# Kernel tuning notes

Measured on AMD Instinct MI355X. Metric: run time of the kernel, lower is better.

Reference implementation:

```python
import jax, jax.numpy as jnp
import numpy as np

N = 100000      # nodes
F_IN = 512      # input features
H = 128         # hidden
C = 16          # classes
E = 3200000     # edges
K = 10          # propagation hops (lg_k == gg_k == 10)
ALPHA = 0.1


def ppr_temp(K, alpha):
    t = alpha * (1.0 - alpha) ** np.arange(K + 1)
    t[-1] = (1.0 - alpha) ** K
    return jnp.asarray(t, dtype=jnp.float32)


def setup_inputs() -> dict:
    key = jax.random.key(0)
    ks = jax.random.split(key, 8)
    x = jax.random.normal(ks[0], (N, F_IN), dtype=jnp.float32)
    edge_index = jax.random.randint(ks[1], (2, E), 0, N, dtype=jnp.int64)
    # Local branch: kaiming-uniform-ish linears
    W1_l = jax.random.uniform(ks[2], (F_IN, H), jnp.float32, -1.0, 1.0) * np.sqrt(6.0 / F_IN)
    b1_l = jnp.zeros((H,), jnp.float32)
    W2_l = jax.random.uniform(ks[3], (H, C), jnp.float32, -1.0, 1.0) * np.sqrt(6.0 / H)
    b2_l = jnp.zeros((C,), jnp.float32)
    temp_l = ppr_temp(K, ALPHA)
    # Global branch: uniform(-0.1, 0.1) linears
    W1_g = jax.random.uniform(ks[4], (F_IN, H), jnp.float32, -0.1, 0.1)
    b1_g = jnp.zeros((H,), jnp.float32)
    W2_g = jax.random.uniform(ks[5], (H, C), jnp.float32, -0.1, 0.1)
    b2_g = jnp.zeros((C,), jnp.float32)
    temp_g = ppr_temp(K, ALPHA)
    return {"x": x, "edge_index": edge_index,
            "W1_l": W1_l, "b1_l": b1_l, "W2_l": W2_l, "b2_l": b2_l, "temp_l": temp_l,
            "W1_g": W1_g, "b1_g": b1_g, "W2_g": W2_g, "b2_g": b2_g, "temp_g": temp_g}


def gpr_prop(x, edge_index, temp):
    # gcn_norm: add self-loops with weight 1, symmetric normalization
    row = jnp.concatenate([edge_index[0], jnp.arange(N, dtype=edge_index.dtype)])
    col = jnp.concatenate([edge_index[1], jnp.arange(N, dtype=edge_index.dtype)])
    deg = jax.ops.segment_sum(jnp.ones(row.shape[0], x.dtype), col, num_segments=N)
    dis = jnp.where(deg > 0, jax.lax.rsqrt(deg), 0.0).astype(x.dtype)
    norm = dis[row] * dis[col]  # [E+N]

    def step(carry, gamma):
        xc, hid = carry
        # gather-scale-scatter: out[col] += norm * xc[row]
        xn = jax.ops.segment_sum(norm[:, None] * xc[row], col, num_segments=N)
        return (xn, hid + gamma * xn), None

    (_, hidden), _ = jax.lax.scan(step, (x, x * temp[0]), temp[1:])
    return hidden


def gprgnn_branch(x, edge_index, W1, b1, W2, b2, temp):
    h1 = jax.nn.relu(x @ W1 + b1)          # [N, H]
    h2 = h1 @ W2 + b2                      # [N, C]
    h2 = gpr_prop(h2, edge_index, temp)    # K-hop GPR diffusion
    return h1, h2, jax.nn.log_softmax(h2, axis=1)


def reference(x, edge_index, W1_l, b1_l, W2_l, b2_l, temp_l,
              W1_g, b1_g, W2_g, b2_g, temp_g):
    h1_l, h2_l, prob_l = gprgnn_branch(x, edge_index, W1_l, b1_l, W2_l, b2_l, temp_l)
    h1_g, h2_g, prob_g = gprgnn_branch(x, edge_index, W1_g, b1_g, W2_g, b2_g, temp_g)
    return (h1_l, h2_l, prob_l, h1_g, h2_g, prob_g)
```

## Files before the change

kernel.cpp:

```cpp
#include <hip/hip_runtime.h>
#include <stdint.h>

#define F_IN 512
#define HDIM 128
#define CDIM 16
#define KHOPS 10

#define NBMAX 1024
#define CSTR 16
#define CHUNK 8192
#define CH2 32768

typedef __bf16 bf16x8 __attribute__((ext_vector_type(8)));
typedef float f32x4 __attribute__((ext_vector_type(4)));

typedef __attribute__((address_space(3))) unsigned int lds_uint;
typedef const __attribute__((address_space(1))) unsigned int g_uint;

__device__ __forceinline__ void dma16(const void* g, void* l) {
    __builtin_amdgcn_global_load_lds((g_uint*)g, (lds_uint*)l, 16, 0, 0);
}

__device__ __forceinline__ unsigned short f2bf(float f) {
    unsigned int u = __float_as_uint(f);
    u += 0x7FFFu + ((u >> 16) & 1u);
    return (unsigned short)(u >> 16);
}

__device__ __forceinline__ bf16x8 ld_bf8(const unsigned short* p) {
    uint4 u = *reinterpret_cast<const uint4*>(p);
    return __builtin_bit_cast(bf16x8, u);
}


__global__ __launch_bounds__(256) void k_ccount(const int* __restrict__ eidx,
                                                int* __restrict__ ccnt, int E) {
    __shared__ int lh[NBMAX];
    int t = threadIdx.x;
    int base = blockIdx.x * CH2;
    int lim = E - base; if (lim > CH2) lim = CH2;
    for (int i = t; i < NBMAX; i += 256) lh[i] = 0;
    __syncthreads();
    for (int j = t; j < lim; j += 256)
        atomicAdd(&lh[eidx[(size_t)E + base + j] >> 8], 1);
    __syncthreads();
    for (int i = t; i < NBMAX; i += 256) {
        int v = lh[i];
        if (v) atomicAdd(&ccnt[i], v);
    }
}

__global__ void k_cscan(const int* __restrict__ ccnt, int* __restrict__ coffs,
                        int* __restrict__ ccur, int nbuk) {
    __shared__ int sh[256];
    int t = threadIdx.x;
    int i0 = t * 4;
    int v0 = ccnt[i0 + 0], v1 = ccnt[i0 + 1], v2 = ccnt[i0 + 2], v3 = ccnt[i0 + 3];
    int s = v0 + v1 + v2 + v3;
    sh[t] = s;
    __syncthreads();
    for (int d = 1; d < 256; d <<= 1) {
        int x = (t >= d) ? sh[t - d] : 0;
        __syncthreads();
        sh[t] += x;
        __syncthreads();
    }
    int e0 = sh[t] - s;
    int e1 = e0 + v0, e2 = e1 + v1, e3 = e2 + v2;
    coffs[i0 + 0] = e0;
    coffs[i0 + 1] = e1;
    coffs[i0 + 2] = e2;
    coffs[i0 + 3] = e3;
    if (t == 255) coffs[1024] = e3 + v3;
    if (i0 + 0 < nbuk) ccur[(i0 + 0) * CSTR] = e0;
    if (i0 + 1 < nbuk) ccur[(i0 + 1) * CSTR] = e1;
    if (i0 + 2 < nbuk) ccur[(i0 + 2) * CSTR] = e2;
    if (i0 + 3 < nbuk) ccur[(i0 + 3) * CSTR] = e3;
}

__global__ __launch_bounds__(256) void k_part(
    const int* __restrict__ eidx, int* __restrict__ ccur,
    uint2* __restrict__ cedges, int E)
{
    __shared__ int lh[NBMAX];
    __shared__ int loff[NBMAX];
    __shared__ int lcur[NBMAX];
    __shared__ int gbase[NBMAX];
    __shared__ int sh[256];

    int t = threadIdx.x;
    int base = blockIdx.x * CHUNK;
    int lim = E - base; if (lim > CHUNK) lim = CHUNK;

    for (int i = t; i < NBMAX; i += 256) lh[i] = 0;
    __syncthreads();

    for (int j = t; j < lim; j += 256) {
        int c = eidx[(size_t)E + base + j];
        atomicAdd(&lh[c >> 8], 1);
    }
    __syncthreads();

    int i0 = t * 4;
    int v0 = lh[i0 + 0], v1 = lh[i0 + 1], v2 = lh[i0 + 2], v3 = lh[i0 + 3];
    int s = v0 + v1 + v2 + v3;
    sh[t] = s;
    __syncthreads();
    for (int d = 1; d < 256; d <<= 1) {
        int x = (t >= d) ? sh[t - d] : 0;
        __syncthreads();
        sh[t] += x;
        __syncthreads();
    }
    int excl = sh[t] - s;
    loff[i0 + 0] = excl; lcur[i0 + 0] = excl;
    gbase[i0 + 0] = v0 ? atomicAdd(&ccur[(i0 + 0) * CSTR], v0) : 0;
    excl += v0;
    loff[i0 + 1] = excl; lcur[i0 + 1] = excl;
    gbase[i0 + 1] = v1 ? atomicAdd(&ccur[(i0 + 1) * CSTR], v1) : 0;
    excl += v1;
    loff[i0 + 2] = excl; lcur[i0 + 2] = excl;
    gbase[i0 + 2] = v2 ? atomicAdd(&ccur[(i0 + 2) * CSTR], v2) : 0;
    excl += v2;
    loff[i0 + 3] = excl; lcur[i0 + 3] = excl;
    gbase[i0 + 3] = v3 ? atomicAdd(&ccur[(i0 + 3) * CSTR], v3) : 0;
    __syncthreads();

    for (int j = t; j < lim; j += 256) {
        int r = eidx[base + j];
        int c = eidx[(size_t)E + base + j];
        int b = c >> 8;
        int lp = atomicAdd(&lcur[b], 1);
        int gpos = gbase[b] + (lp - loff[b]);
        uint2 u; u.x = (unsigned)r; u.y = (unsigned)c;
        cedges[gpos] = u;
    }
}

__global__ __launch_bounds__(256) void k_fineA(
    const uint2* __restrict__ cedges, const int* __restrict__ coffs,
    int* __restrict__ cnt, float* __restrict__ dis, int* __restrict__ offs, int N)
{
    __shared__ int lh[256];
    __shared__ int sh[256];
    int b = blockIdx.x;
    int t = threadIdx.x;
    int col0 = b << 8;
    int segs = coffs[b];
    int sege = coffs[b + 1];
    lh[t] = 0;
    __syncthreads();
    for (int j = segs + t; j < sege; j += 256)
        atomicAdd(&lh[(int)cedges[j].y - col0], 1);
    __syncthreads();
    int c = lh[t];
    sh[t] = c;
    __syncthreads();
    for (int d = 1; d < 256; d <<= 1) {
        int x = (t >= d) ? sh[t - d] : 0;
        __syncthreads();
        sh[t] += x;
        __syncthreads();
    }
    int excl = sh[t] - c;
    int col = col0 + t;
    if (col < N) {
        cnt[col] = c;
        dis[col] = rsqrtf((float)(c + 1));
        offs[col] = segs + excl;
    }
}

__global__ __launch_bounds__(256) void k_fineB(
    const uint2* __restrict__ cedges, const int* __restrict__ coffs,
    const int* __restrict__ offs, int* __restrict__ srcs, int N)
{
    __shared__ int lcur[256];
    int b = blockIdx.x;
    int col0 = b << 8;
    int t = threadIdx.x;
    int col = col0 + t;
    int segs = coffs[b];
    int sege = coffs[b + 1];
    if (col < N) lcur[t] = offs[col];
    __syncthreads();
    for (int j = segs + t; j < sege; j += 256) {
        uint2 e = cedges[j];
        int li = (int)e.y - col0;
        int pos = atomicAdd(&lcur[li], 1);
        srcs[pos] = (int)e.x;
    }
}


__global__ void k_xbf(const float* __restrict__ x, unsigned short* __restrict__ xbf) {
    size_t i = (size_t)blockIdx.x * 2048 + (size_t)threadIdx.x * 8;
    float4 a = *reinterpret_cast<const float4*>(&x[i]);
    float4 b = *reinterpret_cast<const float4*>(&x[i + 4]);
    unsigned short s[8];
    s[0] = f2bf(a.x); s[1] = f2bf(a.y); s[2] = f2bf(a.z); s[3] = f2bf(a.w);
    s[4] = f2bf(b.x); s[5] = f2bf(b.y); s[6] = f2bf(b.z); s[7] = f2bf(b.w);
    *reinterpret_cast<uint4*>(&xbf[i]) = *reinterpret_cast<uint4*>(s);
}


__global__ void k_w1t(const float* __restrict__ W1l, const float* __restrict__ W1g,
                      unsigned short* __restrict__ W1Tl, unsigned short* __restrict__ W1Tg) {
    const float* W1 = blockIdx.y ? W1g : W1l;
    unsigned short* W1T = blockIdx.y ? W1Tg : W1Tl;
    int idx = blockIdx.x * 256 + threadIdx.x;
    int n = idx >> 6;
    int k0 = (idx & 63) * 8;
    unsigned short tmp[8];
    for (int j = 0; j < 8; j++)
        tmp[j] = f2bf(W1[(size_t)(k0 + j) * HDIM + n]);
    *reinterpret_cast<uint4*>(&W1T[(size_t)n * F_IN + k0]) = *reinterpret_cast<uint4*>(tmp);
}


__global__ __launch_bounds__(256, 4) void k_gemm(
    const unsigned short* __restrict__ xbf,
    const unsigned short* __restrict__ W1Tl, const float* __restrict__ b1l,
    const float* __restrict__ W2l, const float* __restrict__ b2l, const float* __restrict__ tl,
    const unsigned short* __restrict__ W1Tg, const float* __restrict__ b1g,
    const float* __restrict__ W2g, const float* __restrict__ b2g, const float* __restrict__ tg,
    const float* __restrict__ dis,
    float* __restrict__ h1l, float* __restrict__ h1g,
    float* __restrict__ y0, float* __restrict__ hidb, int nNode)
{
    const int br = blockIdx.y;
    const unsigned short* w1t = br ? W1Tg : W1Tl;
    const float* B1 = br ? b1g : b1l;
    const float* W2 = br ? W2g : W2l;
    const float* B2 = br ? b2g : b2l;
    const float* tp = br ? tg : tl;
    float* h1 = br ? h1g : h1l;

    __shared__ __align__(16) unsigned short sm[17408];
    unsigned short* As = sm;
    unsigned short* Bs = sm + 8192;
    unsigned short* Hs = sm;

    const int t = threadIdx.x;
    const int lane = t & 63;
    const int w = t >> 6;
    const int row0 = blockIdx.x * 128;

    f32x4 acc[2][8];
    for (int i = 0; i < 2; i++)
        for (int j = 0; j < 8; j++)
            acc[i][j] = f32x4{0.f, 0.f, 0.f, 0.f};

    const int m16 = lane & 15;
    const int q = lane >> 4;

    for (int k0 = 0; k0 < F_IN; k0 += 64) {
        #pragma unroll
        for (int j = 0; j < 4; j++) {
            int S0 = w * 256 + j * 64;
            int S = S0 + lane;
            int row = S >> 3;
            int cb = (S & 7) ^ (row & 7);
            dma16(&xbf[(size_t)(row0 + row) * F_IN + k0 + cb * 8], &As[(size_t)S0 * 8]);
        }
        #pragma unroll
        for (int j = 0; j < 4; j++) {
            int S0 = w * 256 + j * 64;
            int S = S0 + lane;
            int n = S >> 3;
            int cb = (S & 7) ^ (n & 7);
            dma16(&w1t[(size_t)n * F_IN + k0 + cb * 8], &Bs[(size_t)S0 * 8]);
        }
        __syncthreads();

        #pragma unroll
        for (int ksub = 0; ksub < 2; ksub++) {
            bf16x8 bf[8];
            #pragma unroll
            for (int ns = 0; ns < 8; ns++) {
                int n = ns * 16 + m16;
                int slot = n * 8 + ((ksub * 4 + q) ^ (n & 7));
                bf[ns] = ld_bf8(&Bs[slot * 8]);
            }
            bf16x8 af[2];
            #pragma unroll
            for (int ms = 0; ms < 2; ms++) {
                int row = w * 32 + ms * 16 + m16;
                int slot = row * 8 + ((ksub * 4 + q) ^ (row & 7));
                af[ms] = ld_bf8(&As[slot * 8]);
            }
            #pragma unroll
            for (int ns = 0; ns < 8; ns++)
                #pragma unroll
                for (int ms = 0; ms < 2; ms++)
                    acc[ms][ns] = __builtin_amdgcn_mfma_f32_16x16x32_bf16(af[ms], bf[ns], acc[ms][ns], 0, 0, 0);
        }
        __syncthreads();
    }

    #pragma unroll
    for (int ms = 0; ms < 2; ms++) {
        #pragma unroll
        for (int ns = 0; ns < 8; ns++) {
            int n = ns * 16 + m16;
            float bias = B1[n];
            #pragma unroll
            for (int r = 0; r < 4; r++) {
                int m = w * 32 + ms * 16 + q * 4 + r;
                float v = acc[ms][ns][r] + bias;
                v = v > 0.f ? v : 0.f;
                Hs[m * 136 + n] = f2bf(v);
                int node = row0 + m;
                if (node < nNode) h1[(size_t)node * HDIM + n] = v;
            }
        }
    }
    __syncthreads();

    {
        float t0 = tp[0];
        float bias = B2[m16];
        #pragma unroll
        for (int mi = 0; mi < 2; mi++) {
            int mt = w * 2 + mi;
            f32x4 acc2 = f32x4{bias, bias, bias, bias};
            #pragma unroll
            for (int kb = 0; kb < 4; kb++) {
                bf16x8 hf = ld_bf8(&Hs[(mt * 16 + m16) * 136 + kb * 32 + q * 8]);
                unsigned short wtmp[8];
                #pragma unroll
                for (int j = 0; j < 8; j++)
                    wtmp[j] = f2bf(W2[(size_t)(kb * 32 + q * 8 + j) * CDIM + m16]);
                bf16x8 wf = ld_bf8(wtmp);
                acc2 = __builtin_amdgcn_mfma_f32_16x16x32_bf16(hf, wf, acc2, 0, 0, 0);
            }
            #pragma unroll
            for (int r = 0; r < 4; r++) {
                int node = row0 + mt * 16 + q * 4 + r;
                if (node < nNode) {
                    size_t idx = (size_t)node * 32 + (size_t)br * 16 + m16;
                    float val = acc2[r];
                    y0[idx] = dis[node] * val;
                    hidb[idx] = t0 * val;
                }
            }
        }
    }
}


__global__ __launch_bounds__(256) void k_hop3(
    const float* __restrict__ yin, float* __restrict__ yout,
    float* __restrict__ hidb, const int* __restrict__ srcs,
    const int* __restrict__ offs, const int* __restrict__ cnt,
    const float* __restrict__ dis,
    const float* __restrict__ tl, const float* __restrict__ tg,
    float* __restrict__ h2l, float* __restrict__ pl,
    float* __restrict__ h2g, float* __restrict__ pg,
    int hop, int N, int last)
{
    int t = threadIdx.x;
    int v = blockIdx.x * 32 + (t >> 3);
    int s = t & 7;
    int c4 = s * 4;
    if (v >= N) return;
    int off = offs[v];
    int m = cnt[v];
    float d = dis[v];
    size_t vbase = (size_t)v * 32 + c4;
    float4 acc = *reinterpret_cast<const float4*>(yin + vbase);
    const int* ep = srcs + off;
    int i = 0;
    for (; i + 8 <= m; i += 8) {
        int u[8];
        #pragma unroll
        for (int j = 0; j < 8; j++) u[j] = ep[i + j];
        float4 xs[8];
        #pragma unroll
        for (int j = 0; j < 8; j++)
            xs[j] = *reinterpret_cast<const float4*>(yin + (size_t)u[j] * 32 + c4);
        #pragma unroll
        for (int j = 0; j < 8; j++) {
            acc.x += xs[j].x; acc.y += xs[j].y;
            acc.z += xs[j].z; acc.w += xs[j].w;
        }
    }
    for (; i < m; i++) {
        float4 xs = *reinterpret_cast<const float4*>(yin + (size_t)ep[i] * 32 + c4);
        acc.x += xs.x; acc.y += xs.y; acc.z += xs.z; acc.w += xs.w;
    }
    float4 xn = make_float4(d * acc.x, d * acc.y, d * acc.z, d * acc.w);
    float gamma = (s < 4 ? tl : tg)[hop];
    float4 h = *reinterpret_cast<const float4*>(hidb + vbase);
    h.x = fmaf(gamma, xn.x, h.x);
    h.y = fmaf(gamma, xn.y, h.y);
    h.z = fmaf(gamma, xn.z, h.z);
    h.w = fmaf(gamma, xn.w, h.w);
    if (!last) {
        *reinterpret_cast<float4*>(hidb + vbase) = h;
        *reinterpret_cast<float4*>(yout + vbase) =
            make_float4(d * xn.x, d * xn.y, d * xn.z, d * xn.w);
    } else {
        float mloc = fmaxf(fmaxf(h.x, h.y), fmaxf(h.z, h.w));
        mloc = fmaxf(mloc, __shfl_xor(mloc, 1));
        mloc = fmaxf(mloc, __shfl_xor(mloc, 2));
        float sl = __expf(h.x - mloc) + __expf(h.y - mloc) +
                   __expf(h.z - mloc) + __expf(h.w - mloc);
        sl += __shfl_xor(sl, 1);
        sl += __shfl_xor(sl, 2);
        float lse = mloc + __logf(sl);
        float* h2 = s < 4 ? h2l : h2g;
        float* pp = s < 4 ? pl : pg;
        size_t ob = (size_t)v * 16 + (size_t)(s & 3) * 4;
        *reinterpret_cast<float4*>(h2 + ob) = h;
        *reinterpret_cast<float4*>(pp + ob) =
            make_float4(h.x - lse, h.y - lse, h.z - lse, h.w - lse);
    }
}


extern "C" void kernel_launch(void* const* d_in, const int* in_sizes, int n_in,
                              void* d_out, int out_size, void* d_ws, size_t ws_size,
                              hipStream_t stream)
{
    const float* x   = (const float*)d_in[0];
    const int*   eidx= (const int*)d_in[1];
    const float* W1l = (const float*)d_in[2];
    const float* b1l = (const float*)d_in[3];
    const float* W2l = (const float*)d_in[4];
    const float* b2l = (const float*)d_in[5];
    const float* tl  = (const float*)d_in[6];
    const float* W1g = (const float*)d_in[7];
    const float* b1g = (const float*)d_in[8];
    const float* W2g = (const float*)d_in[9];
    const float* b2g = (const float*)d_in[10];
    const float* tg  = (const float*)d_in[11];

    const int N = in_sizes[0] / F_IN;
    const int E = in_sizes[1] / 2;

    float* out = (float*)d_out;
    float* h1l = out;
    float* h2l = h1l + (size_t)N * HDIM;
    float* pl  = h2l + (size_t)N * CDIM;
    float* h1g = pl  + (size_t)N * CDIM;
    float* h2g = h1g + (size_t)N * HDIM;
    float* pg  = h2g + (size_t)N * CDIM;

    char* ws = (char*)d_ws;
    auto alloc = [&](size_t bytes) -> char* {
        char* p = ws;
        ws += (bytes + 1023) & ~(size_t)1023;
        return p;
    };
    int*   cnt      = (int*)alloc((size_t)N * 4);
    int*   offs     = (int*)alloc((size_t)N * 4);
    int*   ccnt     = (int*)alloc((size_t)(NBMAX + 1) * 4);
    int*   coffs    = (int*)alloc((size_t)(NBMAX + 1) * 4);
    int*   ccur     = (int*)alloc((size_t)NBMAX * CSTR * 4);
    float* dis      = (float*)alloc((size_t)N * 4);
    int*   srcs     = (int*)alloc((size_t)E * 4);
    float* yA       = (float*)alloc((size_t)N * 32 * 4);
    float* yB       = (float*)alloc((size_t)N * 32 * 4);
    float* hidb     = (float*)alloc((size_t)N * 32 * 4);
    unsigned short* W1Tl = (unsigned short*)alloc((size_t)HDIM * F_IN * 2);
    unsigned short* W1Tg = (unsigned short*)alloc((size_t)HDIM * F_IN * 2);
    unsigned short* xbf  = (unsigned short*)alloc((size_t)(N + 256) * F_IN * 2);
    uint2* cedges = (uint2*)xbf;

    hipMemsetAsync(ccnt, 0, (size_t)(NBMAX + 1) * 4, stream);

    int nbuk = (N + 255) / 256;

    k_ccount<<<(E + CH2 - 1) / CH2, 256, 0, stream>>>(eidx, ccnt, E);
    k_cscan<<<1, 256, 0, stream>>>(ccnt, coffs, ccur, nbuk);
    k_part<<<(E + CHUNK - 1) / CHUNK, 256, 0, stream>>>(eidx, ccur, cedges, E);
    k_fineA<<<nbuk, 256, 0, stream>>>(cedges, coffs, cnt, dis, offs, N);
    k_fineB<<<nbuk, 256, 0, stream>>>(cedges, coffs, offs, srcs, N);

    k_xbf<<<(int)(((size_t)N * F_IN) / 2048), 256, 0, stream>>>(x, xbf);
    dim3 gw(32, 2);
    k_w1t<<<gw, 256, 0, stream>>>(W1l, W1g, W1Tl, W1Tg);

    dim3 gg((N + 127) / 128, 2);
    k_gemm<<<gg, 256, 0, stream>>>(xbf, W1Tl, b1l, W2l, b2l, tl,
                                   W1Tg, b1g, W2g, b2g, tg, dis,
                                   h1l, h1g, yA, hidb, N);

    int gh = (N + 31) / 32;
    float* a = yA;
    float* b = yB;
    for (int k = 1; k <= KHOPS; k++) {
        k_hop3<<<gh, 256, 0, stream>>>(a, b, hidb, srcs, offs, cnt, dis,
                                       tl, tg, h2l, pl, h2g, pg, k, N, k == KHOPS);
        float* tmp = a; a = b; b = tmp;
    }
}
```

Measured before the change: 1.117 ms.

## Sort nodes by in-degree within buckets and merge fine CSR kernels

Merges the two fine CSR-building kernels into one and adds a per-256-node counting sort by in-degree, producing a permutation. The hop kernel then processes nodes in degree-sorted order, so the 8-thread groups in a wavefront have similar edge counts and diverge less in the gather loop. The cost is one extra indirection through perm per node per hop, plus scattered writes to output rows.

```diff
diff --git a/kernel.cpp b/kernel.cpp
--- a/kernel.cpp
+++ b/kernel.cpp
@@ -137,18 +137,21 @@
     }
 }
 
-__global__ __launch_bounds__(256) void k_fineA(
+__global__ __launch_bounds__(256) void k_fine(
     const uint2* __restrict__ cedges, const int* __restrict__ coffs,
-    int* __restrict__ cnt, float* __restrict__ dis, int* __restrict__ offs, int N)
+    int* __restrict__ cnt, float* __restrict__ dis, int* __restrict__ offs,
+    int* __restrict__ srcs, int* __restrict__ perm, int N)
 {
     __shared__ int lh[256];
     __shared__ int sh[256];
+    __shared__ int dh[512];
+    __shared__ int lcur[256];
     int b = blockIdx.x;
     int t = threadIdx.x;
     int col0 = b << 8;
     int segs = coffs[b];
     int sege = coffs[b + 1];
-    lh[t] = 0;
+    lh[t] = 0; dh[t] = 0; dh[256 + t] = 0;
     __syncthreads();
     for (int j = segs + t; j < sege; j += 256)
         atomicAdd(&lh[(int)cedges[j].y - col0], 1);
@@ -164,26 +167,33 @@
     }
     int excl = sh[t] - c;
     int col = col0 + t;
+    int key = c < 511 ? c : 511;
     if (col < N) {
         cnt[col] = c;
         dis[col] = rsqrtf((float)(c + 1));
         offs[col] = segs + excl;
-    }
-}
-
-__global__ __launch_bounds__(256) void k_fineB(
-    const uint2* __restrict__ cedges, const int* __restrict__ coffs,
-    const int* __restrict__ offs, int* __restrict__ srcs, int N)
-{
-    __shared__ int lcur[256];
-    int b = blockIdx.x;
-    int col0 = b << 8;
-    int t = threadIdx.x;
-    int col = col0 + t;
-    int segs = coffs[b];
-    int sege = coffs[b + 1];
-    if (col < N) lcur[t] = offs[col];
-    __syncthreads();
+        lcur[t] = segs + excl;
+        atomicAdd(&dh[key], 1);
+    }
+    __syncthreads();
+    int b0 = dh[2 * t], b1 = dh[2 * t + 1];
+    int s2 = b0 + b1;
+    sh[t] = s2;
+    __syncthreads();
+    for (int d = 1; d < 256; d <<= 1) {
+        int x = (t >= d) ? sh[t - d] : 0;
+        __syncthreads();
+        sh[t] += x;
+        __syncthreads();
+    }
+    int e2 = sh[t] - s2;
+    dh[2 * t] = e2;
+    dh[2 * t + 1] = e2 + b0;
+    __syncthreads();
+    if (col < N) {
+        int rank = atomicAdd(&dh[key], 1);
+        perm[col0 + rank] = col;
+    }
     for (int j = segs + t; j < sege; j += 256) {
         uint2 e = cedges[j];
         int li = (int)e.y - col0;
@@ -353,17 +363,18 @@
     const float* __restrict__ yin, float* __restrict__ yout,
     float* __restrict__ hidb, const int* __restrict__ srcs,
     const int* __restrict__ offs, const int* __restrict__ cnt,
-    const float* __restrict__ dis,
+    const float* __restrict__ dis, const int* __restrict__ perm,
     const float* __restrict__ tl, const float* __restrict__ tg,
     float* __restrict__ h2l, float* __restrict__ pl,
     float* __restrict__ h2g, float* __restrict__ pg,
     int hop, int N, int last)
 {
     int t = threadIdx.x;
-    int v = blockIdx.x * 32 + (t >> 3);
+    int vi = blockIdx.x * 32 + (t >> 3);
     int s = t & 7;
     int c4 = s * 4;
-    if (v >= N) return;
+    if (vi >= N) return;
+    int v = perm[vi];
     int off = offs[v];
     int m = cnt[v];
     float d = dis[v];
@@ -455,6 +466,7 @@
     };
     int*   cnt      = (int*)alloc((size_t)N * 4);
     int*   offs     = (int*)alloc((size_t)N * 4);
+    int*   perm     = (int*)alloc((size_t)(N + 256) * 4);
     int*   ccnt     = (int*)alloc((size_t)(NBMAX + 1) * 4);
     int*   coffs    = (int*)alloc((size_t)(NBMAX + 1) * 4);
     int*   ccur     = (int*)alloc((size_t)NBMAX * CSTR * 4);
@@ -475,8 +487,7 @@
     k_ccount<<<(E + CH2 - 1) / CH2, 256, 0, stream>>>(eidx, ccnt, E);
     k_cscan<<<1, 256, 0, stream>>>(ccnt, coffs, ccur, nbuk);
     k_part<<<(E + CHUNK - 1) / CHUNK, 256, 0, stream>>>(eidx, ccur, cedges, E);
-    k_fineA<<<nbuk, 256, 0, stream>>>(cedges, coffs, cnt, dis, offs, N);
-    k_fineB<<<nbuk, 256, 0, stream>>>(cedges, coffs, offs, srcs, N);
+    k_fine<<<nbuk, 256, 0, stream>>>(cedges, coffs, cnt, dis, offs, srcs, perm, N);
 
     k_xbf<<<(int)(((size_t)N * F_IN) / 2048), 256, 0, stream>>>(x, xbf);
     dim3 gw(32, 2);
@@ -491,7 +502,7 @@
     float* a = yA;
     float* b = yB;
     for (int k = 1; k <= KHOPS; k++) {
-        k_hop3<<<gh, 256, 0, stream>>>(a, b, hidb, srcs, offs, cnt, dis,
+        k_hop3<<<gh, 256, 0, stream>>>(a, b, hidb, srcs, offs, cnt, dis, perm,
                                        tl, tg, h2l, pl, h2g, pg, k, N, k == KHOPS);
         float* tmp = a; a = b; b = tmp;
     }
```

Result: slower. 1.232 ms (+10.2%).
